# Optimization experiments

Measured on AMD Instinct MI355X. Metric: run time of the kernel, lower is better.

Reference implementation:

```python
import jax, jax.numpy as jnp
from jax import lax
import numpy as np

B = 8192
NUM_CTX = 300; NUM_STN = 300; NUM_GPE = 20; NUM_GPI = 2; NUM_OUT = 20
FF_DIM = 20; FF_STEPS = 20; STN_ITERS = 50
ETA_GPE = 1.0; ETA_STN = 1.0 / 3.0; ETA_GPI = 0.1
A1 = 1.0; A2 = 1.0; THETAD1 = 0.0; THETAD2 = 0.0
UNITS = (64, 128, 64)

_SPECS = [("vf0", UNITS[0], NUM_CTX), ("vf1", UNITS[1], UNITS[0]), ("vf2", UNITS[2], UNITS[1]), ("vf3", 1, UNITS[2]),
          ("jd1", FF_DIM, NUM_CTX), ("jd2", FF_DIM, NUM_CTX), ("kd1", FF_DIM, NUM_CTX), ("kd2", FF_DIM, NUM_CTX),
          ("sg", NUM_GPE, NUM_STN), ("gs", NUM_STN, NUM_GPE), ("glat", NUM_GPE, NUM_GPE), ("slat", NUM_STN, NUM_STN),
          ("d1gpi", NUM_GPI, FF_DIM), ("stngpi", NUM_GPI, NUM_STN),
          ("ih", 4 * NUM_OUT, NUM_GPI), ("hh", 4 * NUM_OUT, NUM_OUT)]


def _lin_init(k, out_d, in_d):
    kw, kb = jax.random.split(k)
    bound = 1.0 / np.sqrt(in_d)
    w = jax.random.uniform(kw, (out_d, in_d), minval=-bound, maxval=bound, dtype=jnp.float32)
    b = jax.random.uniform(kb, (out_d,), minval=-bound, maxval=bound, dtype=jnp.float32)
    return w, b


def setup_inputs() -> dict:
    key = jax.random.key(0)
    ks = iter(jax.random.split(key, 40))
    inp = {}
    inp["stimulus"] = jax.random.normal(next(ks), (B, NUM_CTX), dtype=jnp.float32)
    inp["deltavf"] = jax.random.normal(next(ks), (B, 1), dtype=jnp.float32)
    inp["hx0"] = jax.random.uniform(next(ks), (B, NUM_OUT), dtype=jnp.float32)
    inp["cx0"] = jax.random.uniform(next(ks), (B, NUM_OUT), dtype=jnp.float32)
    for name, o, i in _SPECS:
        w, b = _lin_init(next(ks), o, i)
        inp["w_" + name] = w
        inp["b_" + name] = b
    return inp


def _lin(x, w, b):
    return x @ w.T + b


def _lstm_cell(x, h, c, w_ih, b_ih, w_hh, b_hh):
    gates = _lin(x, w_ih, b_ih) + _lin(h, w_hh, b_hh)
    i, f, g, o = jnp.split(gates, 4, axis=-1)  # torch LSTMCell gate order
    c_new = jax.nn.sigmoid(f) * c + jax.nn.sigmoid(i) * jnp.tanh(g)
    h_new = jax.nn.sigmoid(o) * jnp.tanh(c_new)
    return h_new, c_new


def reference(stimulus, deltavf, hx0, cx0,
              w_vf0, b_vf0, w_vf1, b_vf1, w_vf2, b_vf2, w_vf3, b_vf3,
              w_jd1, b_jd1, w_jd2, b_jd2, w_kd1, b_kd1, w_kd2, b_kd2,
              w_sg, b_sg, w_gs, b_gs, w_glat, b_glat, w_slat, b_slat,
              w_d1gpi, b_d1gpi, w_stngpi, b_stngpi,
              w_ih, b_ih, w_hh, b_hh):
    bsz = stimulus.shape[0]
    # value function head
    h = jax.nn.relu(_lin(stimulus, w_vf0, b_vf0))
    h = jax.nn.relu(_lin(h, w_vf1, b_vf1))
    h = jax.nn.relu(_lin(h, w_vf2, b_vf2))
    vt = jnp.tanh(_lin(h, w_vf3, b_vf3))  # [B, 1]

    lamd1 = jax.nn.sigmoid(A1 * (deltavf - THETAD1))  # [B, 1]
    lamd2 = jax.nn.sigmoid(A2 * (deltavf - THETAD2))  # [B, 1]

    # loop-invariant striatal drives (computed every iter in torch, same value)
    J_D1 = _lin(stimulus, w_jd1, b_jd1)
    J_D2 = _lin(stimulus, w_jd2, b_jd2)
    K_D1 = _lin(stimulus, w_kd1, b_kd1)
    K_D2 = _lin(stimulus, w_kd2, b_kd2)

    def ff_step(carry, _):
        v1, v2 = carry
        v1 = jax.nn.sigmoid(lamd1 * (J_D1 * (1.0 - v1) + (1.0 - K_D1) * v1))
        v2 = jax.nn.sigmoid(lamd2 * (J_D2 * (1.0 - v2) + (1.0 - K_D2) * v2))
        return (v1, v2), None

    z_ff = jnp.zeros((bsz, FF_DIM), dtype=stimulus.dtype)
    (V_D1, V_D2), _ = lax.scan(ff_step, (z_ff, z_ff), None, length=FF_STEPS)

    V_GPi_DP = _lin(V_D1, w_d1gpi, b_d1gpi)  # [B, num_gpi]

    def stn_step(carry, _):
        xgpe, xstn, vstn, vgpi, hx, cx = carry
        xgpe = xgpe + ETA_GPE * (-xgpe + _lin(vstn, w_sg, b_sg) + _lin(xgpe, w_glat, b_glat) - V_D2)
        xstn = xstn + ETA_STN * (-xstn + _lin(xgpe, w_gs, b_gs) + _lin(vstn, w_slat, b_slat))
        vstn = jnp.tanh(lamd2 * xstn)
        V_GPi_IP = lamd2 * _lin(vstn, w_stngpi, b_stngpi)
        vgpi = vgpi + ETA_GPI * (-vgpi - V_GPi_DP + 2.0 * V_GPi_IP)
        hx, cx = _lstm_cell(-vgpi, hx, cx, w_ih, b_ih, w_hh, b_hh)
        return (xgpe, xstn, vstn, vgpi, hx, cx), None

    carry0 = (jnp.zeros((bsz, NUM_GPE), dtype=stimulus.dtype),
              jnp.zeros((bsz, NUM_STN), dtype=stimulus.dtype),
              jnp.zeros((bsz, NUM_STN), dtype=stimulus.dtype),  # tanh(lamd2*0) = 0
              jnp.zeros((bsz, NUM_GPI), dtype=stimulus.dtype),
              hx0, cx0)
    carry, _ = lax.scan(stn_step, carry0, None, length=STN_ITERS)
    hx = carry[4]
    return hx, vt
```

## Files before the change

### kernel.cpp

```cpp
#include <hip/hip_runtime.h>


typedef _Float16 f16_t;
typedef _Float16 f16x8 __attribute__((ext_vector_type(8)));
typedef _Float16 f16x4 __attribute__((ext_vector_type(4)));
typedef float floatx4 __attribute__((ext_vector_type(4)));
typedef float floatx2 __attribute__((ext_vector_type(2)));

#define BTOT 8192
#define BM   32
#define NTHR 512
#define NBLK 256
#define VSTR 328
#define XST  32

struct Params {
  const float *stimulus, *deltavf, *hx0, *cx0;
  const float *w_vf0, *b_vf0, *w_vf1, *b_vf1, *w_vf2, *b_vf2, *w_vf3, *b_vf3;
  const float *w_jd1, *b_jd1, *w_jd2, *b_jd2, *w_kd1, *b_kd1, *w_kd2, *b_kd2;
  const float *w_sg, *b_sg, *w_gs, *b_gs, *w_glat, *b_glat, *w_slat, *b_slat;
  const float *w_d1gpi, *b_d1gpi, *w_stngpi, *b_stngpi;
  const float *w_ih, *b_ih, *w_hh, *b_hh;
  float* out;
};

struct __align__(16) Smem {
  f16_t vstn[BM * VSTR];
  f16_t xgpe[2][BM * XST];
  f16_t hxf[BM * XST];
  f16_t wB2[21 * 512];
  f16_t wsp[10 * 512];
  f16_t whh[5 * 512];
  union { float h1f[BM * 128]; float scr[3200]; float gates[BM * 80]; } u;
  float h0f[BM * 64];
  float V_D2f[BM * 20];
  float lstmc[20][12];
  float bsumS[304];
  float bsg[20];
  float DPs[BM * 2], vgpis[BM * 2], lamS[BM];
};

__device__ __forceinline__ float rcp_f(float x) { return __builtin_amdgcn_rcpf(x); }
__device__ __forceinline__ float sigm_fast(float x) { return rcp_f(1.f + __expf(-x)); }
__device__ __forceinline__ float tanh_fast(float x) { return 1.f - 2.f * rcp_f(1.f + __expf(2.f * x)); }

__device__ __forceinline__ f16x8 ldfrag(const float* row, int k0, int kmax, bool valid) {
  float4 z = make_float4(0.f, 0.f, 0.f, 0.f);
  int nv = valid ? (kmax - k0) : 0;
  float4 f0 = (nv >= 4) ? *(const float4*)(row + k0) : z;
  float4 f1 = (nv >= 8) ? *(const float4*)(row + k0 + 4) : z;
  f16x8 r;
  r[0] = (f16_t)f0.x; r[1] = (f16_t)f0.y; r[2] = (f16_t)f0.z; r[3] = (f16_t)f0.w;
  r[4] = (f16_t)f1.x; r[5] = (f16_t)f1.y; r[6] = (f16_t)f1.z; r[7] = (f16_t)f1.w;
  return r;
}

__global__ __launch_bounds__(NTHR, 2) void bg_main(Params P) {
  __shared__ Smem S;
  const int tid  = threadIdx.x;
  const int lane = tid & 63;
  const int wv   = tid >> 6;
  const int q    = lane >> 4;
  const int cl   = lane & 15;
  const int row0 = blockIdx.x * BM;
  const floatx4 zf = {0.f, 0.f, 0.f, 0.f};

  if (tid < BM) S.lamS[tid] = sigm_fast(P.deltavf[row0 + tid]);
  for (int i = tid; i < BM * 2; i += NTHR) S.vgpis[i] = 0.f;
  for (int i = tid; i < 2 * BM * XST; i += NTHR) ((f16_t*)S.xgpe)[i] = (f16_t)0.f;
  for (int i = tid; i < BM * XST; i += NTHR) {
    int m = i >> 5, j = i & 31;
    S.hxf[i] = (j < 20) ? (f16_t)P.hx0[row0 * 20 + m * 20 + j] : (f16_t)0.f;
  }
  for (int i = tid; i < BM * VSTR; i += NTHR) S.vstn[i] = (f16_t)0.f;
  for (int i = tid; i < 21 * 512; i += NTHR) {
    int t = i >> 9, l = (i >> 3) & 63, jj = i & 7;
    int c2 = l & 15, k = ((l >> 4) << 3) + jj;
    float v = 0.f;
    if (t < 19) { int n = t * 16 + c2; if (n < 300 && k < 20) v = P.w_gs[n * 20 + k]; }
    else        { int g = (t - 19) * 16 + c2; if (g < 20 && k < 20) v = P.w_glat[g * 20 + k]; }
    S.wB2[i] = (f16_t)v;
  }
  for (int i = tid; i < 10 * 512; i += NTHR) {
    int c = i >> 9, l = (i >> 3) & 63, jj = i & 7;
    int p = l & 15, k = c * 32 + ((l >> 4) << 3) + jj;
    float v = (p < 2 && k < 300) ? P.w_stngpi[p * 300 + k] : 0.f;
    S.wsp[i] = (f16_t)v;
  }
  for (int i = tid; i < 5 * 512; i += NTHR) {
    int t = i >> 9, l = (i >> 3) & 63, jj = i & 7;
    int c2 = l & 15, k = ((l >> 4) << 3) + jj;
    int orig = (c2 & 3) * 20 + 4 * t + (c2 >> 2);
    S.whh[i] = (f16_t)((k < 20) ? P.w_hh[orig * 20 + k] : 0.f);
  }
  for (int i = tid; i < 240; i += NTHR) {
    int j = i / 12, c = i - j * 12;
    float v;
    if (c < 4)      v = P.b_ih[c * 20 + j] + P.b_hh[c * 20 + j];
    else if (c < 8) v = P.w_ih[((c - 4) * 20 + j) * 2 + 0];
    else            v = P.w_ih[((c - 8) * 20 + j) * 2 + 1];
    S.lstmc[j][c] = v;
  }
  for (int i = tid; i < 304; i += NTHR) S.bsumS[i] = (i < 300) ? (P.b_slat[i] + P.b_gs[i]) : 0.f;
  for (int i = tid; i < 20; i += NTHR)  S.bsg[i] = P.b_sg[i] + P.b_glat[i];

  {
    int o = tid & 63, mb = (tid >> 6) * 4;
    const float4* wr = (const float4*)(P.w_vf0 + o * 300);
    float bias = P.b_vf0[o], a[4];
#pragma unroll
    for (int u = 0; u < 4; ++u) a[u] = bias;
    for (int kq = 0; kq < 75; ++kq) {
      float4 w = wr[kq];
#pragma unroll
      for (int u = 0; u < 4; ++u) {
        float4 v = *(const float4*)(P.stimulus + (size_t)(row0 + mb + u) * 300 + kq * 4);
        a[u] = fmaf(v.x, w.x, a[u]); a[u] = fmaf(v.y, w.y, a[u]);
        a[u] = fmaf(v.z, w.z, a[u]); a[u] = fmaf(v.w, w.w, a[u]);
      }
    }
#pragma unroll
    for (int u = 0; u < 4; ++u) S.h0f[(mb + u) * 64 + o] = fmaxf(a[u], 0.f);
  }
  __syncthreads();
  {
    int o = tid & 127, mb = (tid >> 7) * 8;
    const float* wr = P.w_vf1 + o * 64;
    float bias = P.b_vf1[o], a[8];
#pragma unroll
    for (int u = 0; u < 8; ++u) a[u] = bias;
    for (int k = 0; k < 64; ++k) {
      float w = wr[k];
#pragma unroll
      for (int u = 0; u < 8; ++u) a[u] = fmaf(S.h0f[(mb + u) * 64 + k], w, a[u]);
    }
#pragma unroll
    for (int u = 0; u < 8; ++u) S.u.h1f[(mb + u) * 128 + o] = fmaxf(a[u], 0.f);
  }
  __syncthreads();
  {
    int o = tid & 63, mb = (tid >> 6) * 4;
    const float* wr = P.w_vf2 + o * 128;
    float bias = P.b_vf2[o], a[4];
#pragma unroll
    for (int u = 0; u < 4; ++u) a[u] = bias;
    for (int k = 0; k < 128; ++k) {
      float w = wr[k];
#pragma unroll
      for (int u = 0; u < 4; ++u) a[u] = fmaf(S.u.h1f[(mb + u) * 128 + k], w, a[u]);
    }
#pragma unroll
    for (int u = 0; u < 4; ++u) S.h0f[(mb + u) * 64 + o] = fmaxf(a[u], 0.f);
  }
  __syncthreads();
  {
    int oid = tid & 127, mb = (tid >> 7) * 8;
    if (oid < 80) {
      int which = oid / 20, o = oid - which * 20;
      const float *wp, *bp;
      if (which == 0)      { wp = P.w_jd1; bp = P.b_jd1; }
      else if (which == 1) { wp = P.w_jd2; bp = P.b_jd2; }
      else if (which == 2) { wp = P.w_kd1; bp = P.b_kd1; }
      else                 { wp = P.w_kd2; bp = P.b_kd2; }
      float bias = bp[o], a[8];
#pragma unroll
      for (int u = 0; u < 8; ++u) a[u] = bias;
      for (int kq = 0; kq < 75; ++kq) {
        float4 w = *(const float4*)(wp + o * 300 + kq * 4);
#pragma unroll
        for (int u = 0; u < 8; ++u) {
          float4 v = *(const float4*)(P.stimulus + (size_t)(row0 + mb + u) * 300 + kq * 4);
          a[u] = fmaf(v.x, w.x, a[u]); a[u] = fmaf(v.y, w.y, a[u]);
          a[u] = fmaf(v.z, w.z, a[u]); a[u] = fmaf(v.w, w.w, a[u]);
        }
      }
#pragma unroll
      for (int u = 0; u < 8; ++u) S.u.scr[which * 640 + (mb + u) * 20 + o] = a[u];
    }
    if (tid < BM) {
      float a = P.b_vf3[0];
      for (int k = 0; k < 64; ++k) a = fmaf(S.h0f[tid * 64 + k], P.w_vf3[k], a);
      P.out[(size_t)BTOT * 20 + row0 + tid] = tanh_fast(a);
    }
  }
  __syncthreads();
  for (int i = tid; i < BM * 20; i += NTHR) {
    int m = i / 20;
    float j1 = S.u.scr[i],        j2 = S.u.scr[640 + i];
    float k1 = S.u.scr[1280 + i], k2 = S.u.scr[1920 + i];
    float L = S.lamS[m], v1 = 0.f, v2 = 0.f;
    for (int s = 0; s < 20; ++s) {
      v1 = sigm_fast(L * (j1 * (1.f - v1) + (1.f - k1) * v1));
      v2 = sigm_fast(L * (j2 * (1.f - v2) + (1.f - k2) * v2));
    }
    S.u.scr[2560 + i] = v1;
    S.V_D2f[i] = v2;
  }
  __syncthreads();
  if (tid < BM * 2) {
    int m = tid >> 1, p2 = tid & 1;
    float a = P.b_d1gpi[p2];
    for (int o = 0; o < 20; ++o) a = fmaf(S.u.scr[2560 + m * 20 + o], P.w_d1gpi[p2 * 20 + o], a);
    S.DPs[tid] = a;
  }
  __syncthreads();

  f16x8 Ws[3][10];
#pragma unroll
  for (int j = 0; j < 3; ++j) {
    int t = wv + 8 * j;
    if (t < 19) {
      int n = t * 16 + cl;
#pragma unroll
      for (int c = 0; c < 10; ++c)
        Ws[j][c] = ldfrag(P.w_slat + (size_t)(n < 300 ? n : 0) * 300, c * 32 + q * 8, 300, n < 300);
    } else if (t < 21) {
      int g = (t - 19) * 16 + cl;
#pragma unroll
      for (int c = 0; c < 10; ++c)
        Ws[j][c] = ldfrag(P.w_sg + (size_t)(g < 20 ? g : 0) * 300, c * 32 + q * 8, 300, g < 20);
    } else {
      f16x8 z;
#pragma unroll
      for (int e = 0; e < 8; ++e) z[e] = (f16_t)0.f;
#pragma unroll
      for (int c = 0; c < 10; ++c) Ws[j][c] = z;
    }
  }
  const float lam0 = S.lamS[cl], lam1 = S.lamS[cl + 16];
  const float bstn0 = P.b_stngpi[0], bstn1 = P.b_stngpi[1];
  const int e0 = tid,        m0 = e0 / 20, j0 = e0 - m0 * 20;
  const int e1 = tid + NTHR, m1 = e1 / 20, j1 = e1 - m1 * 20;
  const bool hase1 = (tid < BM * 20 - NTHR);
  float cxr0 = P.cx0[row0 * 20 + e0], hxr0 = P.hx0[row0 * 20 + e0];
  float cxr1 = hase1 ? P.cx0[row0 * 20 + e1] : 0.f;
  float hxr1 = hase1 ? P.hx0[row0 * 20 + e1] : 0.f;
  const bool isSgW = (wv == 3 || wv == 4);

  floatx4 acc[3][2];
#pragma unroll
  for (int j = 0; j < 3; ++j) { acc[j][0] = zf; acc[j][1] = zf; }

  for (int it = 0; it < 50; ++it) {
    const int po = it & 1, pn = po ^ 1;
    if (isSgW) { acc[2][0] = zf; acc[2][1] = zf; }

    __builtin_amdgcn_s_setprio(1);
#pragma unroll
    for (int c = 0; c < 10; ++c) {
      f16x8 b0 = *(const f16x8*)&S.vstn[cl * VSTR + c * 32 + q * 8];
      f16x8 b1 = *(const f16x8*)&S.vstn[(16 + cl) * VSTR + c * 32 + q * 8];
#pragma unroll
      for (int j = 0; j < 3; ++j) {
        if (wv + 8 * j < 21) {
          acc[j][0] = __builtin_amdgcn_mfma_f32_16x16x32_f16(Ws[j][c], b0, acc[j][0], 0, 0, 0);
          acc[j][1] = __builtin_amdgcn_mfma_f32_16x16x32_f16(Ws[j][c], b1, acc[j][1], 0, 0, 0);
        }
      }
    }
    __builtin_amdgcn_s_setprio(0);
    if (isSgW) {
      f16x8 Wg = *(const f16x8*)&S.wB2[(wv + 16) * 512 + lane * 8];
      f16x8 g0 = *(const f16x8*)&S.xgpe[po][cl * XST + q * 8];
      f16x8 g1 = *(const f16x8*)&S.xgpe[po][(16 + cl) * XST + q * 8];
      acc[2][0] = __builtin_amdgcn_mfma_f32_16x16x32_f16(Wg, g0, acc[2][0], 0, 0, 0);
      acc[2][1] = __builtin_amdgcn_mfma_f32_16x16x32_f16(Wg, g1, acc[2][1], 0, 0, 0);
      int g0i = (wv - 3) * 16 + q * 4;
      if (g0i < 20) {
        floatx4 bg4 = *(const floatx4*)&S.bsg[g0i];
#pragma unroll
        for (int mf = 0; mf < 2; ++mf) {
          int batch = cl + 16 * mf;
          floatx4 vd4 = *(const floatx4*)&S.V_D2f[batch * 20 + g0i];
          f16x4 pk;
#pragma unroll
          for (int r = 0; r < 4; ++r) pk[r] = (f16_t)(acc[2][mf][r] + bg4[r] - vd4[r]);
          *(f16x4*)&S.xgpe[pn][batch * XST + g0i] = pk;
        }
      }
    }
    __syncthreads();

    {
      f16x8 x0 = *(const f16x8*)&S.xgpe[pn][cl * XST + q * 8];
      f16x8 x1 = *(const f16x8*)&S.xgpe[pn][(16 + cl) * XST + q * 8];
      if (wv < 5) {
        f16x8 Wh = *(const f16x8*)&S.whh[wv * 512 + lane * 8];
        f16x8 h0 = *(const f16x8*)&S.hxf[cl * XST + q * 8];
        f16x8 h1 = *(const f16x8*)&S.hxf[(16 + cl) * XST + q * 8];
        floatx4 gA = __builtin_amdgcn_mfma_f32_16x16x32_f16(Wh, h0, zf, 0, 0, 0);
        floatx4 gB = __builtin_amdgcn_mfma_f32_16x16x32_f16(Wh, h1, zf, 0, 0, 0);
        int gb = wv * 16 + q * 4;
        *(floatx4*)&S.u.gates[cl * 80 + gb] = gA;
        *(floatx4*)&S.u.gates[(cl + 16) * 80 + gb] = gB;
      }
#pragma unroll
      for (int j = 0; j < 3; ++j) {
        int t = wv + 8 * j;
        if (t < 19) {
          f16x8 Wg = *(const f16x8*)&S.wB2[t * 512 + lane * 8];
          acc[j][0] = __builtin_amdgcn_mfma_f32_16x16x32_f16(Wg, x0, acc[j][0], 0, 0, 0);
          acc[j][1] = __builtin_amdgcn_mfma_f32_16x16x32_f16(Wg, x1, acc[j][1], 0, 0, 0);
        }
      }
#pragma unroll
      for (int j = 0; j < 3; ++j) {
        int t = wv + 8 * j;
        if (t < 19) {
          int n0 = t * 16 + q * 4;
          if (!(t == 18 && q == 3)) {
            floatx4 bs4 = *(const floatx4*)&S.bsumS[n0];
#pragma unroll
            for (int mf = 0; mf < 2; ++mf) {
              float lm = mf ? lam1 : lam0;
              f16x4 pk;
#pragma unroll
              for (int r = 0; r < 4; ++r) {
                float tmp = acc[j][mf][r] + bs4[r];
                float xn  = tmp * (1.0f / 3.0f);
                acc[j][mf][r] = tmp * (2.0f / 3.0f);
                pk[r] = (f16_t)tanh_fast(lm * xn);
              }
              *(f16x4*)&S.vstn[(cl + 16 * mf) * VSTR + n0] = pk;
            }
          }
        }
      }
    }
    __syncthreads();

    if (wv == 5) {
      floatx4 ip0 = zf, ip1 = zf;
#pragma unroll
      for (int c = 0; c < 10; ++c) {
        f16x8 Wp = *(const f16x8*)&S.wsp[c * 512 + lane * 8];
        f16x8 b0 = *(const f16x8*)&S.vstn[cl * VSTR + c * 32 + q * 8];
        f16x8 b1 = *(const f16x8*)&S.vstn[(16 + cl) * VSTR + c * 32 + q * 8];
        ip0 = __builtin_amdgcn_mfma_f32_16x16x32_f16(Wp, b0, ip0, 0, 0, 0);
        ip1 = __builtin_amdgcn_mfma_f32_16x16x32_f16(Wp, b1, ip1, 0, 0, 0);
      }
      if (q == 0) {
#pragma unroll
        for (int mf = 0; mf < 2; ++mf) {
          int batch = cl + 16 * mf;
          float lm = mf ? lam1 : lam0;
          floatx2 vg = *(const floatx2*)&S.vgpis[batch * 2];
          floatx2 dp = *(const floatx2*)&S.DPs[batch * 2];
          float ipa = lm * ((mf ? ip1[0] : ip0[0]) + bstn0);
          float ipb = lm * ((mf ? ip1[1] : ip0[1]) + bstn1);
          vg[0] = vg[0] + 0.1f * (-vg[0] - dp[0] + 2.f * ipa);
          vg[1] = vg[1] + 0.1f * (-vg[1] - dp[1] + 2.f * ipb);
          *(floatx2*)&S.vgpis[batch * 2] = vg;
        }
      }
    }
    __syncthreads();

    {
      floatx4 g4 = *(const floatx4*)&S.u.gates[m0 * 80 + j0 * 4];
      floatx4 cb = *(const floatx4*)&S.lstmc[j0][0];
      floatx4 w0 = *(const floatx4*)&S.lstmc[j0][4];
      floatx4 w1 = *(const floatx4*)&S.lstmc[j0][8];
      floatx2 vg = *(const floatx2*)&S.vgpis[m0 * 2];
      float gi = g4[0] + cb[0] - w0[0] * vg[0] - w1[0] * vg[1];
      float gf = g4[1] + cb[1] - w0[1] * vg[0] - w1[1] * vg[1];
      float gg = g4[2] + cb[2] - w0[2] * vg[0] - w1[2] * vg[1];
      float go = g4[3] + cb[3] - w0[3] * vg[0] - w1[3] * vg[1];
      float cn = sigm_fast(gf) * cxr0 + sigm_fast(gi) * tanh_fast(gg);
      cxr0 = cn;
      hxr0 = sigm_fast(go) * tanh_fast(cn);
      S.hxf[m0 * XST + j0] = (f16_t)hxr0;
    }
    if (hase1) {
      floatx4 g4 = *(const floatx4*)&S.u.gates[m1 * 80 + j1 * 4];
      floatx4 cb = *(const floatx4*)&S.lstmc[j1][0];
      floatx4 w0 = *(const floatx4*)&S.lstmc[j1][4];
      floatx4 w1 = *(const floatx4*)&S.lstmc[j1][8];
      floatx2 vg = *(const floatx2*)&S.vgpis[m1 * 2];
      float gi = g4[0] + cb[0] - w0[0] * vg[0] - w1[0] * vg[1];
      float gf = g4[1] + cb[1] - w0[1] * vg[0] - w1[1] * vg[1];
      float gg = g4[2] + cb[2] - w0[2] * vg[0] - w1[2] * vg[1];
      float go = g4[3] + cb[3] - w0[3] * vg[0] - w1[3] * vg[1];
      float cn = sigm_fast(gf) * cxr1 + sigm_fast(gi) * tanh_fast(gg);
      cxr1 = cn;
      hxr1 = sigm_fast(go) * tanh_fast(cn);
      S.hxf[m1 * XST + j1] = (f16_t)hxr1;
    }
  }

  P.out[(size_t)row0 * 20 + e0] = hxr0;
  if (hase1) P.out[(size_t)row0 * 20 + e1] = hxr1;
}

extern "C" void kernel_launch(void* const* d_in, const int* in_sizes, int n_in,
                              void* d_out, int out_size, void* d_ws, size_t ws_size,
                              hipStream_t stream) {
  (void)in_sizes; (void)n_in; (void)out_size; (void)d_ws; (void)ws_size;
  Params P;
  P.stimulus = (const float*)d_in[0];
  P.deltavf  = (const float*)d_in[1];
  P.hx0 = (const float*)d_in[2];
  P.cx0 = (const float*)d_in[3];
  P.w_vf0 = (const float*)d_in[4];  P.b_vf0 = (const float*)d_in[5];
  P.w_vf1 = (const float*)d_in[6];  P.b_vf1 = (const float*)d_in[7];
  P.w_vf2 = (const float*)d_in[8];  P.b_vf2 = (const float*)d_in[9];
  P.w_vf3 = (const float*)d_in[10]; P.b_vf3 = (const float*)d_in[11];
  P.w_jd1 = (const float*)d_in[12]; P.b_jd1 = (const float*)d_in[13];
  P.w_jd2 = (const float*)d_in[14]; P.b_jd2 = (const float*)d_in[15];
  P.w_kd1 = (const float*)d_in[16]; P.b_kd1 = (const float*)d_in[17];
  P.w_kd2 = (const float*)d_in[18]; P.b_kd2 = (const float*)d_in[19];
  P.w_sg  = (const float*)d_in[20]; P.b_sg  = (const float*)d_in[21];
  P.w_gs  = (const float*)d_in[22]; P.b_gs  = (const float*)d_in[23];
  P.w_glat= (const float*)d_in[24]; P.b_glat= (const float*)d_in[25];
  P.w_slat= (const float*)d_in[26]; P.b_slat= (const float*)d_in[27];
  P.w_d1gpi  = (const float*)d_in[28]; P.b_d1gpi  = (const float*)d_in[29];
  P.w_stngpi = (const float*)d_in[30]; P.b_stngpi = (const float*)d_in[31];
  P.w_ih = (const float*)d_in[32]; P.b_ih = (const float*)d_in[33];
  P.w_hh = (const float*)d_in[34]; P.b_hh = (const float*)d_in[35];
  P.out  = (float*)d_out;
  bg_main<<<NBLK, NTHR, 0, stream>>>(P);
}
```

Measured before the change: 408.2 us.

## Software-pipeline the STN loop across two half-batch tiles to cut barriers

The 32-row tile is split into two 16-row halves, and each iteration's four phases are staggered across them. The phases are the slat/sg MFMA, the xgpe/gs update with tanh, the GPi projection, and the LSTM cell. Work on one half now overlaps a dependent phase on the other half, and each iteration needs three block barriers instead of four. The LSTM ownership is remapped so each thread handles the same column for both halves. The trade-off is less MFMA independence inside each phase and a pipeline prologue and epilogue.

Measured after the change: 411.9 us. Within noise of the previous version (+0.9%).

```diff
diff --git a/kernel.cpp b/kernel.cpp
--- a/kernel.cpp
+++ b/kernel.cpp
@@ -13,6 +13,8 @@
 #define NBLK 256
 #define VSTR 328
 #define XST  32
+
+template<int N> struct IC { static constexpr int v = N; };
 
 struct Params {
   const float *stimulus, *deltavf, *hx0, *cx0;
@@ -229,167 +231,152 @@
   }
   const float lam0 = S.lamS[cl], lam1 = S.lamS[cl + 16];
   const float bstn0 = P.b_stngpi[0], bstn1 = P.b_stngpi[1];
-  const int e0 = tid,        m0 = e0 / 20, j0 = e0 - m0 * 20;
-  const int e1 = tid + NTHR, m1 = e1 / 20, j1 = e1 - m1 * 20;
-  const bool hase1 = (tid < BM * 20 - NTHR);
-  float cxr0 = P.cx0[row0 * 20 + e0], hxr0 = P.hx0[row0 * 20 + e0];
-  float cxr1 = hase1 ? P.cx0[row0 * 20 + e1] : 0.f;
-  float hxr1 = hase1 ? P.hx0[row0 * 20 + e1] : 0.f;
   const bool isSgW = (wv == 3 || wv == 4);
+  const bool lown = (tid < BM * 20 / 2);
+  const int  m0 = lown ? tid / 20 : 0;
+  const int  j0 = tid - m0 * 20;
+  float cxr0_ = lown ? P.cx0[(size_t)(row0 + m0) * 20 + j0] : 0.f;
+  float cxr1_ = lown ? P.cx0[(size_t)(row0 + 16 + m0) * 20 + j0] : 0.f;
+  float hxr0_ = 0.f, hxr1_ = 0.f;
 
   floatx4 acc[3][2];
 #pragma unroll
   for (int j = 0; j < 3; ++j) { acc[j][0] = zf; acc[j][1] = zf; }
 
-  for (int it = 0; it < 50; ++it) {
+  auto phaseA = [&](auto Hc, int it) {
+    constexpr int H = decltype(Hc)::v;
     const int po = it & 1, pn = po ^ 1;
-    if (isSgW) { acc[2][0] = zf; acc[2][1] = zf; }
-
+    const int br = H * 16 + cl;
+    if (isSgW) acc[2][H] = zf;
     __builtin_amdgcn_s_setprio(1);
 #pragma unroll
     for (int c = 0; c < 10; ++c) {
-      f16x8 b0 = *(const f16x8*)&S.vstn[cl * VSTR + c * 32 + q * 8];
-      f16x8 b1 = *(const f16x8*)&S.vstn[(16 + cl) * VSTR + c * 32 + q * 8];
+      f16x8 b0 = *(const f16x8*)&S.vstn[br * VSTR + c * 32 + q * 8];
 #pragma unroll
       for (int j = 0; j < 3; ++j) {
-        if (wv + 8 * j < 21) {
-          acc[j][0] = __builtin_amdgcn_mfma_f32_16x16x32_f16(Ws[j][c], b0, acc[j][0], 0, 0, 0);
-          acc[j][1] = __builtin_amdgcn_mfma_f32_16x16x32_f16(Ws[j][c], b1, acc[j][1], 0, 0, 0);
-        }
+        if (wv + 8 * j < 21)
+          acc[j][H] = __builtin_amdgcn_mfma_f32_16x16x32_f16(Ws[j][c], b0, acc[j][H], 0, 0, 0);
       }
     }
     __builtin_amdgcn_s_setprio(0);
     if (isSgW) {
       f16x8 Wg = *(const f16x8*)&S.wB2[(wv + 16) * 512 + lane * 8];
-      f16x8 g0 = *(const f16x8*)&S.xgpe[po][cl * XST + q * 8];
-      f16x8 g1 = *(const f16x8*)&S.xgpe[po][(16 + cl) * XST + q * 8];
-      acc[2][0] = __builtin_amdgcn_mfma_f32_16x16x32_f16(Wg, g0, acc[2][0], 0, 0, 0);
-      acc[2][1] = __builtin_amdgcn_mfma_f32_16x16x32_f16(Wg, g1, acc[2][1], 0, 0, 0);
+      f16x8 g0 = *(const f16x8*)&S.xgpe[po][br * XST + q * 8];
+      acc[2][H] = __builtin_amdgcn_mfma_f32_16x16x32_f16(Wg, g0, acc[2][H], 0, 0, 0);
       int g0i = (wv - 3) * 16 + q * 4;
       if (g0i < 20) {
         floatx4 bg4 = *(const floatx4*)&S.bsg[g0i];
-#pragma unroll
-        for (int mf = 0; mf < 2; ++mf) {
-          int batch = cl + 16 * mf;
-          floatx4 vd4 = *(const floatx4*)&S.V_D2f[batch * 20 + g0i];
+        floatx4 vd4 = *(const floatx4*)&S.V_D2f[br * 20 + g0i];
+        f16x4 pk;
+#pragma unroll
+        for (int r = 0; r < 4; ++r) pk[r] = (f16_t)(acc[2][H][r] + bg4[r] - vd4[r]);
+        *(f16x4*)&S.xgpe[pn][br * XST + g0i] = pk;
+      }
+    }
+  };
+
+  auto phaseB = [&](auto Hc, int it) {
+    constexpr int H = decltype(Hc)::v;
+    const int pn = (it & 1) ^ 1;
+    const int br = H * 16 + cl;
+    f16x8 x0 = *(const f16x8*)&S.xgpe[pn][br * XST + q * 8];
+    if (wv < 5) {
+      f16x8 Wh = *(const f16x8*)&S.whh[wv * 512 + lane * 8];
+      f16x8 hv = *(const f16x8*)&S.hxf[br * XST + q * 8];
+      floatx4 gA = __builtin_amdgcn_mfma_f32_16x16x32_f16(Wh, hv, zf, 0, 0, 0);
+      *(floatx4*)&S.u.gates[br * 80 + wv * 16 + q * 4] = gA;
+    }
+#pragma unroll
+    for (int j = 0; j < 3; ++j) {
+      int t = wv + 8 * j;
+      if (t < 19) {
+        f16x8 Wg = *(const f16x8*)&S.wB2[t * 512 + lane * 8];
+        acc[j][H] = __builtin_amdgcn_mfma_f32_16x16x32_f16(Wg, x0, acc[j][H], 0, 0, 0);
+      }
+    }
+    const float lm = H ? lam1 : lam0;
+#pragma unroll
+    for (int j = 0; j < 3; ++j) {
+      int t = wv + 8 * j;
+      if (t < 19) {
+        int n0 = t * 16 + q * 4;
+        if (!(t == 18 && q == 3)) {
+          floatx4 bs4 = *(const floatx4*)&S.bsumS[n0];
           f16x4 pk;
 #pragma unroll
-          for (int r = 0; r < 4; ++r) pk[r] = (f16_t)(acc[2][mf][r] + bg4[r] - vd4[r]);
-          *(f16x4*)&S.xgpe[pn][batch * XST + g0i] = pk;
+          for (int r = 0; r < 4; ++r) {
+            float tmp = acc[j][H][r] + bs4[r];
+            float xn  = tmp * (1.0f / 3.0f);
+            acc[j][H][r] = tmp * (2.0f / 3.0f);
+            pk[r] = (f16_t)tanh_fast(lm * xn);
+          }
+          *(f16x4*)&S.vstn[br * VSTR + n0] = pk;
         }
       }
     }
-    __syncthreads();
-
-    {
-      f16x8 x0 = *(const f16x8*)&S.xgpe[pn][cl * XST + q * 8];
-      f16x8 x1 = *(const f16x8*)&S.xgpe[pn][(16 + cl) * XST + q * 8];
-      if (wv < 5) {
-        f16x8 Wh = *(const f16x8*)&S.whh[wv * 512 + lane * 8];
-        f16x8 h0 = *(const f16x8*)&S.hxf[cl * XST + q * 8];
-        f16x8 h1 = *(const f16x8*)&S.hxf[(16 + cl) * XST + q * 8];
-        floatx4 gA = __builtin_amdgcn_mfma_f32_16x16x32_f16(Wh, h0, zf, 0, 0, 0);
-        floatx4 gB = __builtin_amdgcn_mfma_f32_16x16x32_f16(Wh, h1, zf, 0, 0, 0);
-        int gb = wv * 16 + q * 4;
-        *(floatx4*)&S.u.gates[cl * 80 + gb] = gA;
-        *(floatx4*)&S.u.gates[(cl + 16) * 80 + gb] = gB;
-      }
-#pragma unroll
-      for (int j = 0; j < 3; ++j) {
-        int t = wv + 8 * j;
-        if (t < 19) {
-          f16x8 Wg = *(const f16x8*)&S.wB2[t * 512 + lane * 8];
-          acc[j][0] = __builtin_amdgcn_mfma_f32_16x16x32_f16(Wg, x0, acc[j][0], 0, 0, 0);
-          acc[j][1] = __builtin_amdgcn_mfma_f32_16x16x32_f16(Wg, x1, acc[j][1], 0, 0, 0);
-        }
-      }
-#pragma unroll
-      for (int j = 0; j < 3; ++j) {
-        int t = wv + 8 * j;
-        if (t < 19) {
-          int n0 = t * 16 + q * 4;
-          if (!(t == 18 && q == 3)) {
-            floatx4 bs4 = *(const floatx4*)&S.bsumS[n0];
-#pragma unroll
-            for (int mf = 0; mf < 2; ++mf) {
-              float lm = mf ? lam1 : lam0;
-              f16x4 pk;
-#pragma unroll
-              for (int r = 0; r < 4; ++r) {
-                float tmp = acc[j][mf][r] + bs4[r];
-                float xn  = tmp * (1.0f / 3.0f);
-                acc[j][mf][r] = tmp * (2.0f / 3.0f);
-                pk[r] = (f16_t)tanh_fast(lm * xn);
-              }
-              *(f16x4*)&S.vstn[(cl + 16 * mf) * VSTR + n0] = pk;
-            }
-          }
-        }
-      }
-    }
-    __syncthreads();
-
+  };
+
+  auto phaseC = [&](auto Hc) {
+    constexpr int H = decltype(Hc)::v;
     if (wv == 5) {
-      floatx4 ip0 = zf, ip1 = zf;
+      const int br = H * 16 + cl;
+      floatx4 ip0 = zf;
 #pragma unroll
       for (int c = 0; c < 10; ++c) {
         f16x8 Wp = *(const f16x8*)&S.wsp[c * 512 + lane * 8];
-        f16x8 b0 = *(const f16x8*)&S.vstn[cl * VSTR + c * 32 + q * 8];
-        f16x8 b1 = *(const f16x8*)&S.vstn[(16 + cl) * VSTR + c * 32 + q * 8];
+        f16x8 b0 = *(const f16x8*)&S.vstn[br * VSTR + c * 32 + q * 8];
         ip0 = __builtin_amdgcn_mfma_f32_16x16x32_f16(Wp, b0, ip0, 0, 0, 0);
-        ip1 = __builtin_amdgcn_mfma_f32_16x16x32_f16(Wp, b1, ip1, 0, 0, 0);
       }
       if (q == 0) {
-#pragma unroll
-        for (int mf = 0; mf < 2; ++mf) {
-          int batch = cl + 16 * mf;
-          float lm = mf ? lam1 : lam0;
-          floatx2 vg = *(const floatx2*)&S.vgpis[batch * 2];
-          floatx2 dp = *(const floatx2*)&S.DPs[batch * 2];
-          float ipa = lm * ((mf ? ip1[0] : ip0[0]) + bstn0);
-          float ipb = lm * ((mf ? ip1[1] : ip0[1]) + bstn1);
-          vg[0] = vg[0] + 0.1f * (-vg[0] - dp[0] + 2.f * ipa);
-          vg[1] = vg[1] + 0.1f * (-vg[1] - dp[1] + 2.f * ipb);
-          *(floatx2*)&S.vgpis[batch * 2] = vg;
-        }
-      }
-    }
-    __syncthreads();
-
-    {
-      floatx4 g4 = *(const floatx4*)&S.u.gates[m0 * 80 + j0 * 4];
+        const float lm = H ? lam1 : lam0;
+        floatx2 vg = *(const floatx2*)&S.vgpis[br * 2];
+        floatx2 dp = *(const floatx2*)&S.DPs[br * 2];
+        float ipa = lm * (ip0[0] + bstn0);
+        float ipb = lm * (ip0[1] + bstn1);
+        vg[0] = vg[0] + 0.1f * (-vg[0] - dp[0] + 2.f * ipa);
+        vg[1] = vg[1] + 0.1f * (-vg[1] - dp[1] + 2.f * ipb);
+        *(floatx2*)&S.vgpis[br * 2] = vg;
+      }
+    }
+  };
+
+  auto phaseD = [&](auto Hc, float& cxr, float& hxr) {
+    constexpr int H = decltype(Hc)::v;
+    if (lown) {
+      const int br = H * 16 + m0;
+      floatx4 g4 = *(const floatx4*)&S.u.gates[br * 80 + j0 * 4];
       floatx4 cb = *(const floatx4*)&S.lstmc[j0][0];
       floatx4 w0 = *(const floatx4*)&S.lstmc[j0][4];
       floatx4 w1 = *(const floatx4*)&S.lstmc[j0][8];
-      floatx2 vg = *(const floatx2*)&S.vgpis[m0 * 2];
+      floatx2 vg = *(const floatx2*)&S.vgpis[br * 2];
       float gi = g4[0] + cb[0] - w0[0] * vg[0] - w1[0] * vg[1];
       float gf = g4[1] + cb[1] - w0[1] * vg[0] - w1[1] * vg[1];
       float gg = g4[2] + cb[2] - w0[2] * vg[0] - w1[2] * vg[1];
       float go = g4[3] + cb[3] - w0[3] * vg[0] - w1[3] * vg[1];
-      float cn = sigm_fast(gf) * cxr0 + sigm_fast(gi) * tanh_fast(gg);
-      cxr0 = cn;
-      hxr0 = sigm_fast(go) * tanh_fast(cn);
-      S.hxf[m0 * XST + j0] = (f16_t)hxr0;
-    }
-    if (hase1) {
-      floatx4 g4 = *(const floatx4*)&S.u.gates[m1 * 80 + j1 * 4];
-      floatx4 cb = *(const floatx4*)&S.lstmc[j1][0];
-      floatx4 w0 = *(const floatx4*)&S.lstmc[j1][4];
-      floatx4 w1 = *(const floatx4*)&S.lstmc[j1][8];
-      floatx2 vg = *(const floatx2*)&S.vgpis[m1 * 2];
-      float gi = g4[0] + cb[0] - w0[0] * vg[0] - w1[0] * vg[1];
-      float gf = g4[1] + cb[1] - w0[1] * vg[0] - w1[1] * vg[1];
-      float gg = g4[2] + cb[2] - w0[2] * vg[0] - w1[2] * vg[1];
-      float go = g4[3] + cb[3] - w0[3] * vg[0] - w1[3] * vg[1];
-      float cn = sigm_fast(gf) * cxr1 + sigm_fast(gi) * tanh_fast(gg);
-      cxr1 = cn;
-      hxr1 = sigm_fast(go) * tanh_fast(cn);
-      S.hxf[m1 * XST + j1] = (f16_t)hxr1;
-    }
-  }
-
-  P.out[(size_t)row0 * 20 + e0] = hxr0;
-  if (hase1) P.out[(size_t)row0 * 20 + e1] = hxr1;
+      float cn = sigm_fast(gf) * cxr + sigm_fast(gi) * tanh_fast(gg);
+      cxr = cn;
+      hxr = sigm_fast(go) * tanh_fast(cn);
+      S.hxf[br * XST + j0] = (f16_t)hxr;
+    }
+  };
+
+  for (int g = 0; g <= 50; ++g) {
+    const bool run = (g < 50), ran = (g > 0);
+    if (run) phaseA(IC<0>{}, g);
+    if (ran) phaseC(IC<1>{});
+    if (ran) phaseD(IC<0>{}, cxr0_, hxr0_);
+    __syncthreads();
+    if (run) { phaseB(IC<0>{}, g); phaseA(IC<1>{}, g); }
+    if (ran) phaseD(IC<1>{}, cxr1_, hxr1_);
+    __syncthreads();
+    if (run) { phaseC(IC<0>{}); phaseB(IC<1>{}, g); }
+    __syncthreads();
+  }
+
+  if (lown) {
+    P.out[(size_t)(row0 + m0) * 20 + j0]      = hxr0_;
+    P.out[(size_t)(row0 + 16 + m0) * 20 + j0] = hxr1_;
+  }
 }
 
 extern "C" void kernel_launch(void* const* d_in, const int* in_sizes, int n_in,
```

## Halve batch tile to 16 rows and stream slat/sg fragments from workspace

Applied to the files above, without the earlier changes.

Cuts rows per block from 32 to 16, doubling the grid to 512 blocks and raising launch bounds to 4 blocks per CU. Only the first slat fragment set stays in registers; the other two are pre-packed to f16 MFMA layout by a new prep kernel into the workspace and read from global or cache every iteration. This aims to relieve register pressure and raise occupancy. The costs are that each weight fragment now feeds only one 16-row MFMA, and there are repeated global loads inside the 50-step loop plus an extra launch.

After: 485.3 us. +18.9%, slower.

```diff
diff --git a/kernel.cpp b/kernel.cpp
--- a/kernel.cpp
+++ b/kernel.cpp
@@ -8,11 +8,12 @@
 typedef float floatx2 __attribute__((ext_vector_type(2)));
 
 #define BTOT 8192
-#define BM   32
+#define BM   16
 #define NTHR 512
-#define NBLK 256
+#define NBLK (BTOT / BM)
 #define VSTR 328
 #define XST  32
+#define NFRAG (21 * 10 * 512)
 
 struct Params {
   const float *stimulus, *deltavf, *hx0, *cx0;
@@ -21,6 +22,7 @@
   const float *w_sg, *b_sg, *w_gs, *b_gs, *w_glat, *b_glat, *w_slat, *b_slat;
   const float *w_d1gpi, *b_d1gpi, *w_stngpi, *b_stngpi;
   const float *w_ih, *b_ih, *w_hh, *b_hh;
+  const f16_t* wfrag;
   float* out;
 };
 
@@ -31,7 +33,7 @@
   f16_t wB2[21 * 512];
   f16_t wsp[10 * 512];
   f16_t whh[5 * 512];
-  union { float h1f[BM * 128]; float scr[3200]; float gates[BM * 80]; } u;
+  union { float h1f[BM * 128]; float scr[1600]; float gates[BM * 80]; } u;
   float h0f[BM * 64];
   float V_D2f[BM * 20];
   float lstmc[20][12];
@@ -44,9 +46,9 @@
 __device__ __forceinline__ float sigm_fast(float x) { return rcp_f(1.f + __expf(-x)); }
 __device__ __forceinline__ float tanh_fast(float x) { return 1.f - 2.f * rcp_f(1.f + __expf(2.f * x)); }
 
-__device__ __forceinline__ f16x8 ldfrag(const float* row, int k0, int kmax, bool valid) {
+__device__ __forceinline__ f16x8 ldfrag(const float* row, int k0, int kmax) {
   float4 z = make_float4(0.f, 0.f, 0.f, 0.f);
-  int nv = valid ? (kmax - k0) : 0;
+  int nv = kmax - k0;
   float4 f0 = (nv >= 4) ? *(const float4*)(row + k0) : z;
   float4 f1 = (nv >= 8) ? *(const float4*)(row + k0 + 4) : z;
   f16x8 r;
@@ -55,7 +57,22 @@
   return r;
 }
 
-__global__ __launch_bounds__(NTHR, 2) void bg_main(Params P) {
+__global__ void prep_frags(const float* __restrict__ slat,
+                           const float* __restrict__ sg,
+                           f16_t* __restrict__ dst) {
+  int i = blockIdx.x * blockDim.x + threadIdx.x;
+  if (i >= NFRAG) return;
+  int t = i / 5120, rem = i - t * 5120;
+  int c = rem >> 9, l2 = (rem >> 3) & 63, jj = i & 7;
+  int cl = l2 & 15, q = l2 >> 4;
+  int k = c * 32 + q * 8 + jj;
+  float v = 0.f;
+  if (t < 19) { int n = t * 16 + cl; if (n < 300 && k < 300) v = slat[n * 300 + k]; }
+  else        { int g = (t - 19) * 16 + cl; if (g < 20 && k < 300) v = sg[(size_t)g * 300 + k]; }
+  dst[i] = (f16_t)v;
+}
+
+__global__ __launch_bounds__(NTHR, 4) void bg_main(Params P) {
   __shared__ Smem S;
   const int tid  = threadIdx.x;
   const int lane = tid & 63;
@@ -70,7 +87,7 @@
   for (int i = tid; i < 2 * BM * XST; i += NTHR) ((f16_t*)S.xgpe)[i] = (f16_t)0.f;
   for (int i = tid; i < BM * XST; i += NTHR) {
     int m = i >> 5, j = i & 31;
-    S.hxf[i] = (j < 20) ? (f16_t)P.hx0[row0 * 20 + m * 20 + j] : (f16_t)0.f;
+    S.hxf[i] = (j < 20) ? (f16_t)P.hx0[(size_t)(row0 + m) * 20 + j] : (f16_t)0.f;
   }
   for (int i = tid; i < BM * VSTR; i += NTHR) S.vstn[i] = (f16_t)0.f;
   for (int i = tid; i < 21 * 512; i += NTHR) {
@@ -105,56 +122,54 @@
   for (int i = tid; i < 20; i += NTHR)  S.bsg[i] = P.b_sg[i] + P.b_glat[i];
 
   {
-    int o = tid & 63, mb = (tid >> 6) * 4;
+    int o = tid & 63, mb = (tid >> 6) * 2;
     const float4* wr = (const float4*)(P.w_vf0 + o * 300);
-    float bias = P.b_vf0[o], a[4];
-#pragma unroll
-    for (int u = 0; u < 4; ++u) a[u] = bias;
+    float bias = P.b_vf0[o], a[2];
+    a[0] = bias; a[1] = bias;
     for (int kq = 0; kq < 75; ++kq) {
       float4 w = wr[kq];
 #pragma unroll
-      for (int u = 0; u < 4; ++u) {
+      for (int u = 0; u < 2; ++u) {
         float4 v = *(const float4*)(P.stimulus + (size_t)(row0 + mb + u) * 300 + kq * 4);
         a[u] = fmaf(v.x, w.x, a[u]); a[u] = fmaf(v.y, w.y, a[u]);
         a[u] = fmaf(v.z, w.z, a[u]); a[u] = fmaf(v.w, w.w, a[u]);
       }
     }
 #pragma unroll
-    for (int u = 0; u < 4; ++u) S.h0f[(mb + u) * 64 + o] = fmaxf(a[u], 0.f);
-  }
-  __syncthreads();
-  {
-    int o = tid & 127, mb = (tid >> 7) * 8;
+    for (int u = 0; u < 2; ++u) S.h0f[(mb + u) * 64 + o] = fmaxf(a[u], 0.f);
+  }
+  __syncthreads();
+  {
+    int o = tid & 127, mb = (tid >> 7) * 4;
     const float* wr = P.w_vf1 + o * 64;
-    float bias = P.b_vf1[o], a[8];
-#pragma unroll
-    for (int u = 0; u < 8; ++u) a[u] = bias;
+    float bias = P.b_vf1[o], a[4];
+#pragma unroll
+    for (int u = 0; u < 4; ++u) a[u] = bias;
     for (int k = 0; k < 64; ++k) {
       float w = wr[k];
 #pragma unroll
-      for (int u = 0; u < 8; ++u) a[u] = fmaf(S.h0f[(mb + u) * 64 + k], w, a[u]);
-    }
-#pragma unroll
-    for (int u = 0; u < 8; ++u) S.u.h1f[(mb + u) * 128 + o] = fmaxf(a[u], 0.f);
-  }
-  __syncthreads();
-  {
-    int o = tid & 63, mb = (tid >> 6) * 4;
+      for (int u = 0; u < 4; ++u) a[u] = fmaf(S.h0f[(mb + u) * 64 + k], w, a[u]);
+    }
+#pragma unroll
+    for (int u = 0; u < 4; ++u) S.u.h1f[(mb + u) * 128 + o] = fmaxf(a[u], 0.f);
+  }
+  __syncthreads();
+  {
+    int o = tid & 63, mb = (tid >> 6) * 2;
     const float* wr = P.w_vf2 + o * 128;
-    float bias = P.b_vf2[o], a[4];
-#pragma unroll
-    for (int u = 0; u < 4; ++u) a[u] = bias;
+    float bias = P.b_vf2[o], a[2];
+    a[0] = bias; a[1] = bias;
     for (int k = 0; k < 128; ++k) {
       float w = wr[k];
 #pragma unroll
-      for (int u = 0; u < 4; ++u) a[u] = fmaf(S.u.h1f[(mb + u) * 128 + k], w, a[u]);
-    }
-#pragma unroll
-    for (int u = 0; u < 4; ++u) S.h0f[(mb + u) * 64 + o] = fmaxf(a[u], 0.f);
-  }
-  __syncthreads();
-  {
-    int oid = tid & 127, mb = (tid >> 7) * 8;
+      for (int u = 0; u < 2; ++u) a[u] = fmaf(S.u.h1f[(mb + u) * 128 + k], w, a[u]);
+    }
+#pragma unroll
+    for (int u = 0; u < 2; ++u) S.h0f[(mb + u) * 64 + o] = fmaxf(a[u], 0.f);
+  }
+  __syncthreads();
+  {
+    int oid = tid & 127, mb = (tid >> 7) * 4;
     if (oid < 80) {
       int which = oid / 20, o = oid - which * 20;
       const float *wp, *bp;
@@ -162,20 +177,20 @@
       else if (which == 1) { wp = P.w_jd2; bp = P.b_jd2; }
       else if (which == 2) { wp = P.w_kd1; bp = P.b_kd1; }
       else                 { wp = P.w_kd2; bp = P.b_kd2; }
-      float bias = bp[o], a[8];
-#pragma unroll
-      for (int u = 0; u < 8; ++u) a[u] = bias;
+      float bias = bp[o], a[4];
+#pragma unroll
+      for (int u = 0; u < 4; ++u) a[u] = bias;
       for (int kq = 0; kq < 75; ++kq) {
         float4 w = *(const float4*)(wp + o * 300 + kq * 4);
 #pragma unroll
-        for (int u = 0; u < 8; ++u) {
+        for (int u = 0; u < 4; ++u) {
           float4 v = *(const float4*)(P.stimulus + (size_t)(row0 + mb + u) * 300 + kq * 4);
           a[u] = fmaf(v.x, w.x, a[u]); a[u] = fmaf(v.y, w.y, a[u]);
           a[u] = fmaf(v.z, w.z, a[u]); a[u] = fmaf(v.w, w.w, a[u]);
         }
       }
 #pragma unroll
-      for (int u = 0; u < 8; ++u) S.u.scr[which * 640 + (mb + u) * 20 + o] = a[u];
+      for (int u = 0; u < 4; ++u) S.u.scr[which * 320 + (mb + u) * 20 + o] = a[u];
     }
     if (tid < BM) {
       float a = P.b_vf3[0];
@@ -186,121 +201,95 @@
   __syncthreads();
   for (int i = tid; i < BM * 20; i += NTHR) {
     int m = i / 20;
-    float j1 = S.u.scr[i],        j2 = S.u.scr[640 + i];
-    float k1 = S.u.scr[1280 + i], k2 = S.u.scr[1920 + i];
+    float j1 = S.u.scr[i],       j2 = S.u.scr[320 + i];
+    float k1 = S.u.scr[640 + i], k2 = S.u.scr[960 + i];
     float L = S.lamS[m], v1 = 0.f, v2 = 0.f;
     for (int s = 0; s < 20; ++s) {
       v1 = sigm_fast(L * (j1 * (1.f - v1) + (1.f - k1) * v1));
       v2 = sigm_fast(L * (j2 * (1.f - v2) + (1.f - k2) * v2));
     }
-    S.u.scr[2560 + i] = v1;
+    S.u.scr[1280 + i] = v1;
     S.V_D2f[i] = v2;
   }
   __syncthreads();
   if (tid < BM * 2) {
     int m = tid >> 1, p2 = tid & 1;
     float a = P.b_d1gpi[p2];
-    for (int o = 0; o < 20; ++o) a = fmaf(S.u.scr[2560 + m * 20 + o], P.w_d1gpi[p2 * 20 + o], a);
+    for (int o = 0; o < 20; ++o) a = fmaf(S.u.scr[1280 + m * 20 + o], P.w_d1gpi[p2 * 20 + o], a);
     S.DPs[tid] = a;
   }
   __syncthreads();
 
-  f16x8 Ws[3][10];
-#pragma unroll
-  for (int j = 0; j < 3; ++j) {
-    int t = wv + 8 * j;
-    if (t < 19) {
-      int n = t * 16 + cl;
-#pragma unroll
-      for (int c = 0; c < 10; ++c)
-        Ws[j][c] = ldfrag(P.w_slat + (size_t)(n < 300 ? n : 0) * 300, c * 32 + q * 8, 300, n < 300);
-    } else if (t < 21) {
-      int g = (t - 19) * 16 + cl;
-#pragma unroll
-      for (int c = 0; c < 10; ++c)
-        Ws[j][c] = ldfrag(P.w_sg + (size_t)(g < 20 ? g : 0) * 300, c * 32 + q * 8, 300, g < 20);
-    } else {
-      f16x8 z;
-#pragma unroll
-      for (int e = 0; e < 8; ++e) z[e] = (f16_t)0.f;
-#pragma unroll
-      for (int c = 0; c < 10; ++c) Ws[j][c] = z;
-    }
-  }
-  const float lam0 = S.lamS[cl], lam1 = S.lamS[cl + 16];
+  f16x8 Ws0[10];
+  {
+    int n = wv * 16 + cl;
+    const float* a0 = P.w_slat + (size_t)n * 300;
+#pragma unroll
+    for (int c = 0; c < 10; ++c) Ws0[c] = ldfrag(a0, c * 32 + q * 8, 300);
+  }
+  const f16x8* __restrict__ WG = (const f16x8*)P.wfrag;
+  const int t1 = 8 + wv;
+  const int t2 = 16 + wv;
+  const bool has2 = (wv < 5);
+  const bool isSgW = (wv == 3 || wv == 4);
+  const float lamB = S.lamS[cl];
   const float bstn0 = P.b_stngpi[0], bstn1 = P.b_stngpi[1];
-  const int e0 = tid,        m0 = e0 / 20, j0 = e0 - m0 * 20;
-  const int e1 = tid + NTHR, m1 = e1 / 20, j1 = e1 - m1 * 20;
-  const bool hase1 = (tid < BM * 20 - NTHR);
-  float cxr0 = P.cx0[row0 * 20 + e0], hxr0 = P.hx0[row0 * 20 + e0];
-  float cxr1 = hase1 ? P.cx0[row0 * 20 + e1] : 0.f;
-  float hxr1 = hase1 ? P.hx0[row0 * 20 + e1] : 0.f;
-  const bool isSgW = (wv == 3 || wv == 4);
-
-  floatx4 acc[3][2];
-#pragma unroll
-  for (int j = 0; j < 3; ++j) { acc[j][0] = zf; acc[j][1] = zf; }
+  const bool lown = (tid < BM * 20);
+  const int  m0 = lown ? tid / 20 : 0;
+  const int  j0 = tid - m0 * 20;
+  float cxr0 = lown ? P.cx0[(size_t)(row0 + m0) * 20 + j0] : 0.f;
+  float hxr0 = 0.f;
+
+  floatx4 acc[3];
+  acc[0] = zf; acc[1] = zf; acc[2] = zf;
 
   for (int it = 0; it < 50; ++it) {
     const int po = it & 1, pn = po ^ 1;
-    if (isSgW) { acc[2][0] = zf; acc[2][1] = zf; }
+    if (isSgW) acc[2] = zf;
 
     __builtin_amdgcn_s_setprio(1);
 #pragma unroll
     for (int c = 0; c < 10; ++c) {
       f16x8 b0 = *(const f16x8*)&S.vstn[cl * VSTR + c * 32 + q * 8];
-      f16x8 b1 = *(const f16x8*)&S.vstn[(16 + cl) * VSTR + c * 32 + q * 8];
-#pragma unroll
-      for (int j = 0; j < 3; ++j) {
-        if (wv + 8 * j < 21) {
-          acc[j][0] = __builtin_amdgcn_mfma_f32_16x16x32_f16(Ws[j][c], b0, acc[j][0], 0, 0, 0);
-          acc[j][1] = __builtin_amdgcn_mfma_f32_16x16x32_f16(Ws[j][c], b1, acc[j][1], 0, 0, 0);
-        }
+      acc[0] = __builtin_amdgcn_mfma_f32_16x16x32_f16(Ws0[c], b0, acc[0], 0, 0, 0);
+      f16x8 a1 = WG[(t1 * 10 + c) * 64 + lane];
+      acc[1] = __builtin_amdgcn_mfma_f32_16x16x32_f16(a1, b0, acc[1], 0, 0, 0);
+      if (has2) {
+        f16x8 a2 = WG[(t2 * 10 + c) * 64 + lane];
+        acc[2] = __builtin_amdgcn_mfma_f32_16x16x32_f16(a2, b0, acc[2], 0, 0, 0);
       }
     }
     __builtin_amdgcn_s_setprio(0);
     if (isSgW) {
       f16x8 Wg = *(const f16x8*)&S.wB2[(wv + 16) * 512 + lane * 8];
       f16x8 g0 = *(const f16x8*)&S.xgpe[po][cl * XST + q * 8];
-      f16x8 g1 = *(const f16x8*)&S.xgpe[po][(16 + cl) * XST + q * 8];
-      acc[2][0] = __builtin_amdgcn_mfma_f32_16x16x32_f16(Wg, g0, acc[2][0], 0, 0, 0);
-      acc[2][1] = __builtin_amdgcn_mfma_f32_16x16x32_f16(Wg, g1, acc[2][1], 0, 0, 0);
+      acc[2] = __builtin_amdgcn_mfma_f32_16x16x32_f16(Wg, g0, acc[2], 0, 0, 0);
       int g0i = (wv - 3) * 16 + q * 4;
       if (g0i < 20) {
         floatx4 bg4 = *(const floatx4*)&S.bsg[g0i];
-#pragma unroll
-        for (int mf = 0; mf < 2; ++mf) {
-          int batch = cl + 16 * mf;
-          floatx4 vd4 = *(const floatx4*)&S.V_D2f[batch * 20 + g0i];
-          f16x4 pk;
-#pragma unroll
-          for (int r = 0; r < 4; ++r) pk[r] = (f16_t)(acc[2][mf][r] + bg4[r] - vd4[r]);
-          *(f16x4*)&S.xgpe[pn][batch * XST + g0i] = pk;
-        }
+        floatx4 vd4 = *(const floatx4*)&S.V_D2f[cl * 20 + g0i];
+        f16x4 pk;
+#pragma unroll
+        for (int r = 0; r < 4; ++r) pk[r] = (f16_t)(acc[2][r] + bg4[r] - vd4[r]);
+        *(f16x4*)&S.xgpe[pn][cl * XST + g0i] = pk;
       }
     }
     __syncthreads();
 
     {
       f16x8 x0 = *(const f16x8*)&S.xgpe[pn][cl * XST + q * 8];
-      f16x8 x1 = *(const f16x8*)&S.xgpe[pn][(16 + cl) * XST + q * 8];
       if (wv < 5) {
         f16x8 Wh = *(const f16x8*)&S.whh[wv * 512 + lane * 8];
-        f16x8 h0 = *(const f16x8*)&S.hxf[cl * XST + q * 8];
-        f16x8 h1 = *(const f16x8*)&S.hxf[(16 + cl) * XST + q * 8];
-        floatx4 gA = __builtin_amdgcn_mfma_f32_16x16x32_f16(Wh, h0, zf, 0, 0, 0);
-        floatx4 gB = __builtin_amdgcn_mfma_f32_16x16x32_f16(Wh, h1, zf, 0, 0, 0);
-        int gb = wv * 16 + q * 4;
-        *(floatx4*)&S.u.gates[cl * 80 + gb] = gA;
-        *(floatx4*)&S.u.gates[(cl + 16) * 80 + gb] = gB;
+        f16x8 hv = *(const f16x8*)&S.hxf[cl * XST + q * 8];
+        floatx4 gA = __builtin_amdgcn_mfma_f32_16x16x32_f16(Wh, hv, zf, 0, 0, 0);
+        *(floatx4*)&S.u.gates[cl * 80 + wv * 16 + q * 4] = gA;
       }
 #pragma unroll
       for (int j = 0; j < 3; ++j) {
         int t = wv + 8 * j;
         if (t < 19) {
           f16x8 Wg = *(const f16x8*)&S.wB2[t * 512 + lane * 8];
-          acc[j][0] = __builtin_amdgcn_mfma_f32_16x16x32_f16(Wg, x0, acc[j][0], 0, 0, 0);
-          acc[j][1] = __builtin_amdgcn_mfma_f32_16x16x32_f16(Wg, x1, acc[j][1], 0, 0, 0);
+          acc[j] = __builtin_amdgcn_mfma_f32_16x16x32_f16(Wg, x0, acc[j], 0, 0, 0);
         }
       }
 #pragma unroll
@@ -310,19 +299,15 @@
           int n0 = t * 16 + q * 4;
           if (!(t == 18 && q == 3)) {
             floatx4 bs4 = *(const floatx4*)&S.bsumS[n0];
-#pragma unroll
-            for (int mf = 0; mf < 2; ++mf) {
-              float lm = mf ? lam1 : lam0;
-              f16x4 pk;
-#pragma unroll
-              for (int r = 0; r < 4; ++r) {
-                float tmp = acc[j][mf][r] + bs4[r];
-                float xn  = tmp * (1.0f / 3.0f);
-                acc[j][mf][r] = tmp * (2.0f / 3.0f);
-                pk[r] = (f16_t)tanh_fast(lm * xn);
-              }
-              *(f16x4*)&S.vstn[(cl + 16 * mf) * VSTR + n0] = pk;
+            f16x4 pk;
+#pragma unroll
+            for (int r = 0; r < 4; ++r) {
+              float tmp = acc[j][r] + bs4[r];
+              float xn  = tmp * (1.0f / 3.0f);
+              acc[j][r] = tmp * (2.0f / 3.0f);
+              pk[r] = (f16_t)tanh_fast(lamB * xn);
             }
+            *(f16x4*)&S.vstn[cl * VSTR + n0] = pk;
           }
         }
       }
@@ -330,33 +315,26 @@
     __syncthreads();
 
     if (wv == 5) {
-      floatx4 ip0 = zf, ip1 = zf;
+      floatx4 ip0 = zf;
 #pragma unroll
       for (int c = 0; c < 10; ++c) {
         f16x8 Wp = *(const f16x8*)&S.wsp[c * 512 + lane * 8];
         f16x8 b0 = *(const f16x8*)&S.vstn[cl * VSTR + c * 32 + q * 8];
-        f16x8 b1 = *(const f16x8*)&S.vstn[(16 + cl) * VSTR + c * 32 + q * 8];
         ip0 = __builtin_amdgcn_mfma_f32_16x16x32_f16(Wp, b0, ip0, 0, 0, 0);
-        ip1 = __builtin_amdgcn_mfma_f32_16x16x32_f16(Wp, b1, ip1, 0, 0, 0);
       }
       if (q == 0) {
-#pragma unroll
-        for (int mf = 0; mf < 2; ++mf) {
-          int batch = cl + 16 * mf;
-          float lm = mf ? lam1 : lam0;
-          floatx2 vg = *(const floatx2*)&S.vgpis[batch * 2];
-          floatx2 dp = *(const floatx2*)&S.DPs[batch * 2];
-          float ipa = lm * ((mf ? ip1[0] : ip0[0]) + bstn0);
-          float ipb = lm * ((mf ? ip1[1] : ip0[1]) + bstn1);
-          vg[0] = vg[0] + 0.1f * (-vg[0] - dp[0] + 2.f * ipa);
-          vg[1] = vg[1] + 0.1f * (-vg[1] - dp[1] + 2.f * ipb);
-          *(floatx2*)&S.vgpis[batch * 2] = vg;
-        }
+        floatx2 vg = *(const floatx2*)&S.vgpis[cl * 2];
+        floatx2 dp = *(const floatx2*)&S.DPs[cl * 2];
+        float ipa = lamB * (ip0[0] + bstn0);
+        float ipb = lamB * (ip0[1] + bstn1);
+        vg[0] = vg[0] + 0.1f * (-vg[0] - dp[0] + 2.f * ipa);
+        vg[1] = vg[1] + 0.1f * (-vg[1] - dp[1] + 2.f * ipb);
+        *(floatx2*)&S.vgpis[cl * 2] = vg;
       }
     }
     __syncthreads();
 
-    {
+    if (lown) {
       floatx4 g4 = *(const floatx4*)&S.u.gates[m0 * 80 + j0 * 4];
       floatx4 cb = *(const floatx4*)&S.lstmc[j0][0];
       floatx4 w0 = *(const floatx4*)&S.lstmc[j0][4];
@@ -371,31 +349,15 @@
       hxr0 = sigm_fast(go) * tanh_fast(cn);
       S.hxf[m0 * XST + j0] = (f16_t)hxr0;
     }
-    if (hase1) {
-      floatx4 g4 = *(const floatx4*)&S.u.gates[m1 * 80 + j1 * 4];
-      floatx4 cb = *(const floatx4*)&S.lstmc[j1][0];
-      floatx4 w0 = *(const floatx4*)&S.lstmc[j1][4];
-      floatx4 w1 = *(const floatx4*)&S.lstmc[j1][8];
-      floatx2 vg = *(const floatx2*)&S.vgpis[m1 * 2];
-      float gi = g4[0] + cb[0] - w0[0] * vg[0] - w1[0] * vg[1];
-      float gf = g4[1] + cb[1] - w0[1] * vg[0] - w1[1] * vg[1];
-      float gg = g4[2] + cb[2] - w0[2] * vg[0] - w1[2] * vg[1];
-      float go = g4[3] + cb[3] - w0[3] * vg[0] - w1[3] * vg[1];
-      float cn = sigm_fast(gf) * cxr1 + sigm_fast(gi) * tanh_fast(gg);
-      cxr1 = cn;
-      hxr1 = sigm_fast(go) * tanh_fast(cn);
-      S.hxf[m1 * XST + j1] = (f16_t)hxr1;
-    }
-  }
-
-  P.out[(size_t)row0 * 20 + e0] = hxr0;
-  if (hase1) P.out[(size_t)row0 * 20 + e1] = hxr1;
+  }
+
+  if (lown) P.out[(size_t)(row0 + m0) * 20 + j0] = hxr0;
 }
 
 extern "C" void kernel_launch(void* const* d_in, const int* in_sizes, int n_in,
                               void* d_out, int out_size, void* d_ws, size_t ws_size,
                               hipStream_t stream) {
-  (void)in_sizes; (void)n_in; (void)out_size; (void)d_ws; (void)ws_size;
+  (void)in_sizes; (void)n_in; (void)out_size; (void)ws_size;
   Params P;
   P.stimulus = (const float*)d_in[0];
   P.deltavf  = (const float*)d_in[1];
@@ -417,6 +379,8 @@
   P.w_stngpi = (const float*)d_in[30]; P.b_stngpi = (const float*)d_in[31];
   P.w_ih = (const float*)d_in[32]; P.b_ih = (const float*)d_in[33];
   P.w_hh = (const float*)d_in[34]; P.b_hh = (const float*)d_in[35];
+  P.wfrag = (const f16_t*)d_ws;
   P.out  = (float*)d_out;
+  prep_frags<<<(NFRAG + 511) / 512, 512, 0, stream>>>(P.w_slat, P.w_sg, (f16_t*)d_ws);
   bg_main<<<NBLK, NTHR, 0, stream>>>(P);
 }
```
